# Kernel tuning notes

Hardware: AMD Instinct MI355X
Metric: run time of the kernel (lower is better)

Reference implementation:

```python
import jax, jax.numpy as jnp
import numpy as np

B, S, D = 2, 4096, 2048
HQ, HK, HV = 32, 8, 8
H = max(HQ, HK, HV)
DK, DV = 64, 64
OUT = 2048
CHUNK = 64  # chunked-recurrent block size


def setup_inputs() -> dict:
    key = jax.random.key(0)
    k1, k2, k3 = jax.random.split(key, 3)
    x = jax.random.normal(k1, (B, S, D), dtype=jnp.float32)
    input_state = jnp.zeros((B, H * DK * DV), dtype=jnp.float32)
    qkv = HQ * DK + HK * DK + HV * DV  # 3072
    # Linear weights stored as [in, out]; equals torch weight.T so y = x @ W
    W_in = jax.random.normal(k2, (D, qkv), dtype=jnp.float32) * (D ** -0.5)
    W_out = jax.random.normal(k3, (H * DV, OUT), dtype=jnp.float32) * ((H * DV) ** -0.5)
    return {"x": x, "input_state": input_state, "W_in": W_in, "W_out": W_out}


def _linear_attention(q, k, v, S0):
    # q,k,v: [B,S,H,d]; S0: [B,H,DK,DV]
    nc = S // CHUNK
    # move chunk axis to front for lax.scan: [nc, B, CHUNK, H, d]
    qc = jnp.moveaxis(q.reshape(B, nc, CHUNK, H, DK), 1, 0)
    kc = jnp.moveaxis(k.reshape(B, nc, CHUNK, H, DK), 1, 0)
    vc = jnp.moveaxis(v.reshape(B, nc, CHUNK, H, DV), 1, 0)
    mask = jnp.tril(jnp.ones((CHUNK, CHUNK), dtype=bool))  # causal within chunk

    def step(Sstate, blk):
        qb, kb, vb = blk  # [B,C,H,d]
        A = jnp.einsum('bihd,bjhd->bhij', qb, kb)
        A = jnp.where(mask, A, jnp.zeros((), A.dtype))
        o = jnp.einsum('bhij,bjhd->bihd', A, vb) \
            + jnp.einsum('bihd,bhde->bihe', qb, Sstate)
        Sstate = Sstate + jnp.einsum('bjhd,bjhe->bhde', kb, vb)
        return Sstate, o

    Sf, o = jax.lax.scan(step, S0, (qc, kc, vc))
    o = jnp.moveaxis(o, 0, 1).reshape(B, S, H, DV)
    return o, Sf


def reference(x, input_state, W_in, W_out):
    proj = x @ W_in  # [B,S,3072]
    q, k, v = jnp.split(proj, [HQ * DK, HQ * DK + HK * DK], axis=-1)
    q = q.reshape(B, S, HQ, DK)
    k = k.reshape(B, S, HK, DK)
    v = v.reshape(B, S, HV, DV)
    # GQA: repeat kv heads up to num_heads = max(...)
    k = jnp.repeat(k, H // HK, axis=2)
    v = jnp.repeat(v, H // HV, axis=2)
    S0 = input_state.reshape(B, H, DK, DV)
    o, Sf = _linear_attention(q, k, v, S0)
    out = o.reshape(B, S, H * DV) @ W_out
    return out, Sf.reshape(B, H, DK * DV)
```

## Files before the change

### kernel.cpp

```cpp
#include <hip/hip_runtime.h>

typedef __bf16 bf16_t;
typedef __bf16 bf16x8 __attribute__((ext_vector_type(8)));
typedef __bf16 bf16x4 __attribute__((ext_vector_type(4)));
typedef float  f32x4  __attribute__((ext_vector_type(4)));

#define MFMA16(a,b,c) __builtin_amdgcn_mfma_f32_16x16x32_bf16((a),(b),(c),0,0,0)

__device__ __forceinline__ void gl_lds16(const void* g, void* l) {
    __builtin_amdgcn_global_load_lds(
        (__attribute__((address_space(1))) void*)(g),
        (__attribute__((address_space(3))) void*)(l),
        16, 0, 0);
}

static constexpr int S_TOT   = 8192;
static constexpr int D_IN    = 2048;
static constexpr int QKV     = 3072;
static constexpr int OUT_D   = 2048;
static constexpr int NCHUNK  = 64;
static constexpr int ZSTR    = 88;

__global__ __launch_bounds__(256)
void prep(const float* __restrict__ x, bf16_t* __restrict__ xb,
          const float* __restrict__ W_in, bf16_t* __restrict__ WinT,
          const float* __restrict__ W_out, bf16_t* __restrict__ WoutT) {
    __shared__ float tile[64][65];
    const int bid = blockIdx.x;
    const int t   = threadIdx.x;
    if (bid < 16384) {
        int i = bid * 256 + t;
        f32x4 v = ((const f32x4*)x)[i];
        bf16x4 o;
        o[0] = (bf16_t)v[0]; o[1] = (bf16_t)v[1]; o[2] = (bf16_t)v[2]; o[3] = (bf16_t)v[3];
        ((bf16x4*)xb)[i] = o;
        return;
    }
    const float* in; bf16_t* out; int R, C, bx, by;
    int tb = bid - 16384;
    if (tb < 1536) { in = W_in;  out = WinT;  R = 2048; C = 3072; bx = tb % 48; by = tb / 48; }
    else { tb -= 1536; in = W_out; out = WoutT; R = 2048; C = 2048; bx = tb % 32; by = tb / 32; }
    const int r0 = by * 64, c0 = bx * 64;
#pragma unroll
    for (int p = 0; p < 4; p++) {
        int row = p * 16 + (t >> 4);
        int col = (t & 15) * 4;
        f32x4 v = *(const f32x4*)&in[(size_t)(r0 + row) * C + c0 + col];
        tile[row][col + 0] = v[0]; tile[row][col + 1] = v[1];
        tile[row][col + 2] = v[2]; tile[row][col + 3] = v[3];
    }
    __syncthreads();
#pragma unroll
    for (int p = 0; p < 4; p++) {
        int oc  = p * 16 + (t >> 4);
        int orr = (t & 15) * 4;
        bf16x4 v;
        v[0] = (bf16_t)tile[orr + 0][oc]; v[1] = (bf16_t)tile[orr + 1][oc];
        v[2] = (bf16_t)tile[orr + 2][oc]; v[3] = (bf16_t)tile[orr + 3][oc];
        *(bf16x4*)&out[(size_t)(c0 + oc) * R + r0 + orr] = v;
    }
}

template<int OUT_BF16, int NTILE, int NSTRIDE>
__global__ __launch_bounds__(256, 4)
void gemm_bt(const bf16_t* __restrict__ A, const bf16_t* __restrict__ Bt,
             void* __restrict__ Cout, int M, int N, int K) {
    __shared__ alignas(16) bf16_t lA[128 * 32];
    __shared__ alignas(16) bf16_t lB[128 * 32];
    const int tid = threadIdx.x;
    const int m0 = blockIdx.y * 128;
    const int w = tid >> 6, lane = tid & 63;
    const int wr = (w >> 1) * 64, wc = (w & 1) * 64;
    const int l15 = lane & 15, q8 = (lane >> 4) * 8, q4 = (lane >> 4) * 4;
    const bf16_t* Ag = A + (size_t)(m0 + (tid >> 2)) * K + (tid & 3) * 8;
    const size_t rowStep = (size_t)64 * K;
    bf16_t* lA_t = lA + tid * 8;
    bf16_t* lB_t = lB + tid * 8;
#pragma unroll
    for (int tI = 0; tI < NTILE; tI++) {
        const int n0 = (blockIdx.x + tI * NSTRIDE) * 128;
        const bf16_t* Bg = Bt + (size_t)(n0 + (tid >> 2)) * K + (tid & 3) * 8;
        f32x4 acc[4][4] = {};
        for (int k0 = 0; k0 < K; k0 += 32) {
            gl_lds16(Ag + k0,           lA_t);
            gl_lds16(Ag + k0 + rowStep, lA_t + 64 * 32);
            gl_lds16(Bg + k0,           lB_t);
            gl_lds16(Bg + k0 + rowStep, lB_t + 64 * 32);
            __syncthreads();
            bf16x8 bfr[4];
#pragma unroll
            for (int nj = 0; nj < 4; nj++) bfr[nj] = *(const bf16x8*)&lB[(wc + nj * 16 + l15) * 32 + q8];
#pragma unroll
            for (int mi = 0; mi < 4; mi++) {
                bf16x8 afr = *(const bf16x8*)&lA[(wr + mi * 16 + l15) * 32 + q8];
#pragma unroll
                for (int nj = 0; nj < 4; nj++)
                    acc[mi][nj] = MFMA16(afr, bfr[nj], acc[mi][nj]);
            }
            __syncthreads();
        }
        if (OUT_BF16) {
            bf16_t* C = (bf16_t*)Cout;
#pragma unroll
            for (int mi = 0; mi < 4; mi++)
#pragma unroll
                for (int nj = 0; nj < 4; nj++)
#pragma unroll
                    for (int r = 0; r < 4; r++)
                        C[(size_t)(m0 + wr + mi * 16 + q4 + r) * N + n0 + wc + nj * 16 + l15] =
                            (bf16_t)acc[mi][nj][r];
        } else {
            float* C = (float*)Cout;
#pragma unroll
            for (int mi = 0; mi < 4; mi++)
#pragma unroll
                for (int nj = 0; nj < 4; nj++)
#pragma unroll
                    for (int r = 0; r < 4; r++)
                        C[(size_t)(m0 + wr + mi * 16 + q4 + r) * N + n0 + wc + nj * 16 + l15] =
                            acc[mi][nj][r];
        }
    }
}

__global__ __launch_bounds__(64)
void kv_fused(const bf16_t* __restrict__ proj, bf16_t* __restrict__ vT_g,
              float* __restrict__ Zc) {
    const int idx = blockIdx.x;
    const int c = idx & 63, hk = (idx >> 6) & 7, b = idx >> 9;
    const int tokBase = b * 4096 + c * 64;
    __shared__ float tk[64][65];
    __shared__ float tv[64][65];
    const int lane = threadIdx.x;
    const bf16_t* kg = proj + (size_t)tokBase * QKV + 2048 + hk * 64;
    const bf16_t* vg = proj + (size_t)tokBase * QKV + 2560 + hk * 64;
#pragma unroll
    for (int p = 0; p < 8; p++) {
        int tok = p * 8 + (lane >> 3);
        int d0  = (lane & 7) * 8;
        bf16x8 kv = *(const bf16x8*)&kg[(size_t)tok * QKV + d0];
        bf16x8 vv = *(const bf16x8*)&vg[(size_t)tok * QKV + d0];
#pragma unroll
        for (int e = 0; e < 8; e++) {
            tk[tok][d0 + e] = (float)kv[e];
            tv[tok][d0 + e] = (float)vv[e];
        }
    }
    __syncthreads();
#pragma unroll
    for (int p = 0; p < 8; p++) {
        int dv = p * 8 + (lane >> 3);
        int t0 = (lane & 7) * 8;
        bf16x8 o;
#pragma unroll
        for (int e = 0; e < 8; e++) o[e] = (bf16_t)tv[t0 + e][dv];
        *(bf16x8*)&vT_g[(size_t)idx * 4096 + dv * 64 + t0] = o;
    }
    const int l15 = lane & 15, q8 = (lane >> 4) * 8, q4 = (lane >> 4) * 4;
    f32x4 acc[4][4] = {};
#pragma unroll
    for (int ks = 0; ks < 2; ks++) {
        bf16x8 af[4], bf_[4];
#pragma unroll
        for (int mi = 0; mi < 4; mi++)
#pragma unroll
            for (int e = 0; e < 8; e++) af[mi][e] = (bf16_t)tv[ks * 32 + q8 + e][mi * 16 + l15];
#pragma unroll
        for (int nj = 0; nj < 4; nj++)
#pragma unroll
            for (int e = 0; e < 8; e++) bf_[nj][e] = (bf16_t)tk[ks * 32 + q8 + e][nj * 16 + l15];
#pragma unroll
        for (int mi = 0; mi < 4; mi++)
#pragma unroll
            for (int nj = 0; nj < 4; nj++)
                acc[mi][nj] = MFMA16(af[mi], bf_[nj], acc[mi][nj]);
    }
    float* zout = Zc + (size_t)idx * 4096;
#pragma unroll
    for (int mi = 0; mi < 4; mi++)
#pragma unroll
        for (int nj = 0; nj < 4; nj++)
#pragma unroll
            for (int r = 0; r < 4; r++)
                zout[(mi * 16 + q4 + r) * 64 + nj * 16 + l15] = acc[mi][nj][r];
}

__global__ __launch_bounds__(256)
void prefix_state(const float* __restrict__ Zc, const float* __restrict__ S0,
                  bf16_t* __restrict__ Zp, float* __restrict__ SfOut) {
    const int slice = blockIdx.x & 15;
    const int bh = blockIdx.x >> 4;
    const int h = bh & 31, b = bh >> 5;
    const int hk = h >> 2;
    const int e = slice * 256 + threadIdx.x;
    const int dv = e >> 6, dk = e & 63;
    float acc = S0[(size_t)b * 131072 + h * 4096 + dk * 64 + dv];
    const float* zc = Zc + ((size_t)(b * 8 + hk) * 64) * 4096 + e;
    bf16_t* zp = Zp + ((size_t)(b * 32 + h) * 64) * 4096 + e;
#pragma unroll 4
    for (int c = 0; c < NCHUNK; c++) {
        zp[(size_t)c * 4096] = (bf16_t)acc;
        acc += zc[(size_t)c * 4096];
    }
    SfOut[(size_t)b * 131072 + h * 4096 + dk * 64 + dv] = acc;
}

__global__ __launch_bounds__(256)
void attn_chunk(const bf16_t* __restrict__ proj, const bf16_t* __restrict__ vT_g,
                const bf16_t* __restrict__ Zp, bf16_t* __restrict__ O) {
    const int idx = blockIdx.x;
    const int hk = idx & 7, c = (idx >> 3) & 63, b = idx >> 9;
    const int g = threadIdx.x >> 6, lane = threadIdx.x & 63;
    const int h = hk * 4 + g;
    const int tokBase = b * 4096 + c * 64;
    __shared__ alignas(16) bf16_t zs_all[4][64 * ZSTR];
    bf16_t* zs = zs_all[g];
    const int l15 = lane & 15, q8 = (lane >> 4) * 8, q4 = (lane >> 4) * 4;
    const bf16_t* qrow  = proj + (size_t)tokBase * QKV + h * 64;
    const bf16_t* krow  = proj + (size_t)tokBase * QKV + 2048 + hk * 64;
    const bf16_t* zrow  = Zp + (((size_t)(b * 32 + h)) * 64 + c) * 4096;
    const bf16_t* vTrow = vT_g + ((size_t)(b * 8 + hk) * 64 + c) * 4096;

    bf16x8 qf[2][4];
#pragma unroll
    for (int ks = 0; ks < 2; ks++)
#pragma unroll
        for (int mi = 0; mi < 4; mi++)
            qf[ks][mi] = *(const bf16x8*)&qrow[(size_t)(mi * 16 + l15) * QKV + ks * 32 + q8];

    f32x4 oacc[4][4] = {};
#pragma unroll
    for (int ks = 0; ks < 2; ks++) {
        bf16x8 zf[4];
#pragma unroll
        for (int nj = 0; nj < 4; nj++) zf[nj] = *(const bf16x8*)&zrow[(nj * 16 + l15) * 64 + ks * 32 + q8];
#pragma unroll
        for (int mi = 0; mi < 4; mi++)
#pragma unroll
            for (int nj = 0; nj < 4; nj++)
                oacc[mi][nj] = MFMA16(qf[ks][mi], zf[nj], oacc[mi][nj]);
    }
    f32x4 sacc[4][4] = {};
#pragma unroll
    for (int ks = 0; ks < 2; ks++) {
        bf16x8 kf[4];
#pragma unroll
        for (int nj = 0; nj < 4; nj++) kf[nj] = *(const bf16x8*)&krow[(size_t)(nj * 16 + l15) * QKV + ks * 32 + q8];
#pragma unroll
        for (int mi = 0; mi < 4; mi++)
#pragma unroll
            for (int nj = 0; nj < 4; nj++)
                if (mi >= nj) sacc[mi][nj] = MFMA16(qf[ks][mi], kf[nj], sacc[mi][nj]);
    }
#pragma unroll
    for (int mi = 0; mi < 4; mi++)
#pragma unroll
        for (int nj = 0; nj < 4; nj++)
#pragma unroll
            for (int r = 0; r < 4; r++) {
                int ti = mi * 16 + q4 + r, tj = nj * 16 + l15;
                float v = (ti >= tj) ? sacc[mi][nj][r] : 0.0f;
                zs[ti * ZSTR + tj] = (bf16_t)v;
            }
    __syncthreads();
#pragma unroll
    for (int ks = 0; ks < 2; ks++) {
        bf16x8 sf[4], vf[4];
#pragma unroll
        for (int mi = 0; mi < 4; mi++) sf[mi] = *(const bf16x8*)&zs[(mi * 16 + l15) * ZSTR + ks * 32 + q8];
#pragma unroll
        for (int nj = 0; nj < 4; nj++) vf[nj] = *(const bf16x8*)&vTrow[(nj * 16 + l15) * 64 + ks * 32 + q8];
#pragma unroll
        for (int mi = 0; mi < 4; mi++)
#pragma unroll
            for (int nj = 0; nj < 4; nj++)
                oacc[mi][nj] = MFMA16(sf[mi], vf[nj], oacc[mi][nj]);
    }
    bf16_t* og = O + (size_t)tokBase * OUT_D + h * 64;
#pragma unroll
    for (int mi = 0; mi < 4; mi++)
#pragma unroll
        for (int nj = 0; nj < 4; nj++)
#pragma unroll
            for (int r = 0; r < 4; r++)
                og[(size_t)(mi * 16 + q4 + r) * OUT_D + nj * 16 + l15] = (bf16_t)oacc[mi][nj][r];
}

extern "C" void kernel_launch(void* const* d_in, const int* in_sizes, int n_in,
                              void* d_out, int out_size, void* d_ws, size_t ws_size,
                              hipStream_t stream) {
    const float* x     = (const float*)d_in[0];
    const float* S0    = (const float*)d_in[1];
    const float* W_in  = (const float*)d_in[2];
    const float* W_out = (const float*)d_in[3];

    char* ws = (char*)d_ws;
    bf16_t* xb    = (bf16_t*)(ws + 0);
    bf16_t* WinT  = (bf16_t*)(ws + 33554432);
    bf16_t* WoutT = (bf16_t*)(ws + 46137344);
    bf16_t* proj  = (bf16_t*)(ws + 54525952);
    float*  Zc    = (float*) (ws + 104857600);
    bf16_t* Zp    = (bf16_t*)(ws + 121634816);
    bf16_t* vT_g  = (bf16_t*)(ws + 0);
    bf16_t* Ob    = (bf16_t*)(ws + 8388608);

    float* outMain  = (float*)d_out;
    float* outState = (float*)d_out + (size_t)S_TOT * OUT_D;

    prep<<<16384 + 1536 + 1024, 256, 0, stream>>>(x, xb, W_in, WinT, W_out, WoutT);
    gemm_bt<1, 2, 12><<<dim3(12, 64), 256, 0, stream>>>(xb, WinT, proj, S_TOT, QKV, D_IN);
    kv_fused<<<1024, 64, 0, stream>>>(proj, vT_g, Zc);
    prefix_state<<<1024, 256, 0, stream>>>(Zc, S0, Zp, outState);
    attn_chunk<<<1024, 256, 0, stream>>>(proj, vT_g, Zp, Ob);
    gemm_bt<0, 1, 16><<<dim3(16, 64), 256, 0, stream>>>(Ob, WoutT, outMain, S_TOT, OUT_D, OUT_D);
}
```

Baseline: 423.1 us.

## Deepen GEMM K-tile to 64 with XOR-swizzled LDS and one N-tile per block

The bf16 GEMM now stages a 64-wide K slice per iteration instead of 32, which halves the number of barrier pairs per K loop. Its LDS layout uses an XOR swizzle on the 16-byte column chunks to avoid bank conflicts on fragment reads. The multi-N-tile-per-block loop is removed, and the input projection launches 24x64 blocks with one tile each. LDS per block doubles to 32KB, which may limit occupancy at 4 blocks per CU, and there is still no double buffering.

```diff
diff --git a/kernel.cpp b/kernel.cpp
--- a/kernel.cpp
+++ b/kernel.cpp
@@ -61,65 +61,72 @@
     }
 }
 
-template<int OUT_BF16, int NTILE, int NSTRIDE>
+template<int OUT_BF16>
 __global__ __launch_bounds__(256, 4)
 void gemm_bt(const bf16_t* __restrict__ A, const bf16_t* __restrict__ Bt,
              void* __restrict__ Cout, int M, int N, int K) {
-    __shared__ alignas(16) bf16_t lA[128 * 32];
-    __shared__ alignas(16) bf16_t lB[128 * 32];
+    __shared__ alignas(16) bf16_t lA[128 * 64];
+    __shared__ alignas(16) bf16_t lB[128 * 64];
     const int tid = threadIdx.x;
     const int m0 = blockIdx.y * 128;
+    const int n0 = blockIdx.x * 128;
     const int w = tid >> 6, lane = tid & 63;
     const int wr = (w >> 1) * 64, wc = (w & 1) * 64;
-    const int l15 = lane & 15, q8 = (lane >> 4) * 8, q4 = (lane >> 4) * 4;
-    const bf16_t* Ag = A + (size_t)(m0 + (tid >> 2)) * K + (tid & 3) * 8;
-    const size_t rowStep = (size_t)64 * K;
+    const int l15 = lane & 15, q = lane >> 4, q4 = q * 4;
+    const int trow = tid >> 3;
+    const int tcc  = (tid & 7) ^ (trow & 7);
+    const bf16_t* Ag = A + (size_t)(m0 + trow) * K + tcc * 8;
+    const bf16_t* Bg = Bt + (size_t)(n0 + trow) * K + tcc * 8;
     bf16_t* lA_t = lA + tid * 8;
     bf16_t* lB_t = lB + tid * 8;
-#pragma unroll
-    for (int tI = 0; tI < NTILE; tI++) {
-        const int n0 = (blockIdx.x + tI * NSTRIDE) * 128;
-        const bf16_t* Bg = Bt + (size_t)(n0 + (tid >> 2)) * K + (tid & 3) * 8;
-        f32x4 acc[4][4] = {};
-        for (int k0 = 0; k0 < K; k0 += 32) {
-            gl_lds16(Ag + k0,           lA_t);
-            gl_lds16(Ag + k0 + rowStep, lA_t + 64 * 32);
-            gl_lds16(Bg + k0,           lB_t);
-            gl_lds16(Bg + k0 + rowStep, lB_t + 64 * 32);
-            __syncthreads();
+    const size_t rs = (size_t)32 * K;
+    const int cc0 = (q)     ^ (l15 & 7);
+    const int cc1 = (4 + q) ^ (l15 & 7);
+    f32x4 acc[4][4] = {};
+    for (int k0 = 0; k0 < K; k0 += 64) {
+#pragma unroll
+        for (int j = 0; j < 4; j++) {
+            gl_lds16(Ag + k0 + j * rs, lA_t + j * 2048);
+            gl_lds16(Bg + k0 + j * rs, lB_t + j * 2048);
+        }
+        __syncthreads();
+#pragma unroll
+        for (int ksub = 0; ksub < 2; ksub++) {
+            const int cc = ksub ? cc1 : cc0;
             bf16x8 bfr[4];
 #pragma unroll
-            for (int nj = 0; nj < 4; nj++) bfr[nj] = *(const bf16x8*)&lB[(wc + nj * 16 + l15) * 32 + q8];
+            for (int nj = 0; nj < 4; nj++)
+                bfr[nj] = *(const bf16x8*)&lB[(wc + nj * 16 + l15) * 64 + cc * 8];
 #pragma unroll
             for (int mi = 0; mi < 4; mi++) {
-                bf16x8 afr = *(const bf16x8*)&lA[(wr + mi * 16 + l15) * 32 + q8];
+                bf16x8 afr = *(const bf16x8*)&lA[(wr + mi * 16 + l15) * 64 + cc * 8];
 #pragma unroll
                 for (int nj = 0; nj < 4; nj++)
                     acc[mi][nj] = MFMA16(afr, bfr[nj], acc[mi][nj]);
             }
-            __syncthreads();
         }
-        if (OUT_BF16) {
-            bf16_t* C = (bf16_t*)Cout;
-#pragma unroll
-            for (int mi = 0; mi < 4; mi++)
-#pragma unroll
-                for (int nj = 0; nj < 4; nj++)
-#pragma unroll
-                    for (int r = 0; r < 4; r++)
-                        C[(size_t)(m0 + wr + mi * 16 + q4 + r) * N + n0 + wc + nj * 16 + l15] =
-                            (bf16_t)acc[mi][nj][r];
-        } else {
-            float* C = (float*)Cout;
-#pragma unroll
-            for (int mi = 0; mi < 4; mi++)
-#pragma unroll
-                for (int nj = 0; nj < 4; nj++)
-#pragma unroll
-                    for (int r = 0; r < 4; r++)
-                        C[(size_t)(m0 + wr + mi * 16 + q4 + r) * N + n0 + wc + nj * 16 + l15] =
-                            acc[mi][nj][r];
-        }
+        __syncthreads();
+    }
+    if (OUT_BF16) {
+        bf16_t* C = (bf16_t*)Cout;
+#pragma unroll
+        for (int mi = 0; mi < 4; mi++)
+#pragma unroll
+            for (int nj = 0; nj < 4; nj++)
+#pragma unroll
+                for (int r = 0; r < 4; r++)
+                    C[(size_t)(m0 + wr + mi * 16 + q4 + r) * N + n0 + wc + nj * 16 + l15] =
+                        (bf16_t)acc[mi][nj][r];
+    } else {
+        float* C = (float*)Cout;
+#pragma unroll
+        for (int mi = 0; mi < 4; mi++)
+#pragma unroll
+            for (int nj = 0; nj < 4; nj++)
+#pragma unroll
+                for (int r = 0; r < 4; r++)
+                    C[(size_t)(m0 + wr + mi * 16 + q4 + r) * N + n0 + wc + nj * 16 + l15] =
+                        acc[mi][nj][r];
     }
 }
 
@@ -308,9 +315,9 @@
     float* outState = (float*)d_out + (size_t)S_TOT * OUT_D;
 
     prep<<<16384 + 1536 + 1024, 256, 0, stream>>>(x, xb, W_in, WinT, W_out, WoutT);
-    gemm_bt<1, 2, 12><<<dim3(12, 64), 256, 0, stream>>>(xb, WinT, proj, S_TOT, QKV, D_IN);
+    gemm_bt<1><<<dim3(24, 64), 256, 0, stream>>>(xb, WinT, proj, S_TOT, QKV, D_IN);
     kv_fused<<<1024, 64, 0, stream>>>(proj, vT_g, Zc);
     prefix_state<<<1024, 256, 0, stream>>>(Zc, S0, Zp, outState);
     attn_chunk<<<1024, 256, 0, stream>>>(proj, vT_g, Zp, Ob);
-    gemm_bt<0, 1, 16><<<dim3(16, 64), 256, 0, stream>>>(Ob, WoutT, outMain, S_TOT, OUT_D, OUT_D);
-}
+    gemm_bt<0><<<dim3(16, 64), 256, 0, stream>>>(Ob, WoutT, outMain, S_TOT, OUT_D, OUT_D);
+}
```

After: 371.2 us. 1.14x faster.
